# Kernel optimization log

Measured on AMD Instinct MI355X. Metric: run time of the kernel, lower is better.

## Reference

```python
import jax, jax.numpy as jnp
import numpy as np

N, C, SD, A, H = 1048576, 8192, 32, 4, 64


def _xavier(key, shape):
    fan_in, fan_out = shape
    lim = np.sqrt(6.0 / (fan_in + fan_out)).astype(np.float32)
    return jax.random.uniform(key, shape, jnp.float32, -lim, lim)


def setup_inputs() -> dict:
    key = jax.random.key(0)
    ks = jax.random.split(key, 10)
    return {
        "cell_state": jax.random.normal(ks[0], (N, SD), jnp.float32),
        "arch_state": jax.random.uniform(ks[1], (N, A), jnp.float32),
        "energy": jax.random.uniform(ks[2], (N,), jnp.float32),
        "phi_local": jax.random.uniform(ks[3], (N,), jnp.float32),
        "W1": _xavier(ks[4], (SD + A, H)),
        "b1": jnp.zeros((H,), jnp.float32),
        "W2": _xavier(ks[5], (H, 1)),
        "b2": jnp.zeros((1,), jnp.float32),
        "Wc1": _xavier(ks[6], (A + 3, H // 2)),
        "bc1": jnp.zeros((H // 2,), jnp.float32),
        "Wc2": _xavier(ks[7], (H // 2, 1)),
        "bc2": jnp.zeros((1,), jnp.float32),
        "segment_ids": jnp.sort(jax.random.randint(ks[8], (N,), 0, C, jnp.int32)),
        "n_clusters": C,
    }


def reference(cell_state, arch_state, energy, phi_local,
              W1, b1, W2, b2, Wc1, bc1, Wc2, bc2,
              segment_ids, n_clusters):
    seg = segment_ids
    nc = n_clusters
    seg_sum = lambda v: jax.ops.segment_sum(v, seg, num_segments=nc)

    # ---- cells -> clusters ----
    x = jnp.concatenate([cell_state, arch_state], axis=-1)          # [N, SD+A]
    h = jax.nn.relu(x @ W1 + b1)                                    # [N, H]
    base = jax.nn.sigmoid(h @ W2 + b2)[:, 0]                        # [N]
    importance = jnp.clip(base * energy * phi_local, 0.01, 1.0)
    w = importance * energy * phi_local                              # cell weight

    counts = seg_sum(jnp.ones_like(w))                               # [C]
    wsum = seg_sum(w)                                                # [C]
    safe_cnt = jnp.maximum(counts, 1.0)
    # normalized weights; uniform fallback when a cluster's weight sum is 0
    norm_w = jnp.where(wsum[seg] > 0,
                       w / jnp.maximum(wsum, 1e-30)[seg],
                       1.0 / safe_cnt[seg])
    aggregate = seg_sum(norm_w[:, None] * arch_state)                # [C, A]

    # unbiased per-dim variance averaged over dims (torch .var(dim=0).mean())
    mean = seg_sum(arch_state) / safe_cnt[:, None]                   # [C, A]
    sqdev = seg_sum((arch_state - mean[seg]) ** 2)                   # [C, A]
    var = jnp.where(counts >= 2.0,
                    sqdev.mean(-1) / jnp.maximum(counts - 1.0, 1.0),
                    0.0)                                             # [C]
    phi_cluster = 1.0 - jnp.minimum(1.0, var * 2.0)
    coherence = 1.0 - var

    # ---- clusters -> organism ----
    feats = jnp.concatenate([aggregate,
                             phi_cluster[:, None],
                             coherence[:, None],
                             jnp.minimum(1.0, counts / 20.0)[:, None]], axis=-1)  # [C, A+3]
    hc = jax.nn.relu(feats @ Wc1 + bc1)
    basec = jax.nn.sigmoid(hc @ Wc2 + bc2)[:, 0]                     # [C]
    impc = jnp.clip(basec * phi_cluster, 0.01, 1.0)
    valid = counts > 0
    wc = jnp.where(valid, impc * counts, 0.0)
    wc_sum = wc.sum()
    nvalid = jnp.maximum(valid.sum().astype(jnp.float32), 1.0)
    norm_wc = jnp.where(wc_sum > 0,
                        wc / jnp.maximum(wc_sum, 1e-30),
                        valid.astype(jnp.float32) / nvalid)
    global_archetype = (norm_wc[:, None] * aggregate).sum(0)         # [A]

    return aggregate, phi_cluster, coherence, global_archetype
```

## Files before the change

kernel.cpp:

```cpp
#include <hip/hip_runtime.h>
#include <hip/hip_bf16.h>

#define NC 8192
#define SDIM 32
#define ADIM 4
#define XDIM 36
#define HDIM 64
#define MLP_BLOCKS 1024

typedef _Float16 half8 __attribute__((ext_vector_type(8)));
typedef float f32x4 __attribute__((ext_vector_type(4)));

__device__ __forceinline__ float sigmoidf_(float t) {
    return 1.0f / (1.0f + __expf(-t));
}

__global__ __launch_bounds__(256) void bounds_kernel(
    const int* __restrict__ seg, int* __restrict__ startx,
    int* __restrict__ endx, int n)
{
    const int i = blockIdx.x * 256 + threadIdx.x;
    if (i >= n) return;
    const int s = seg[i];
    if (i == 0) {
        startx[s] = 0;
        for (int c = 0; c < s; ++c) { startx[c] = 0; endx[c] = 0; }
    } else {
        const int sp = seg[i - 1];
        if (sp != s) {
            startx[s] = i;
            for (int c = sp + 1; c < s; ++c) { startx[c] = i; endx[c] = i; }
        }
    }
    if (i == n - 1) {
        endx[s] = n;
        for (int c = s + 1; c < NC; ++c) { startx[c] = n; endx[c] = n; }
    } else if (seg[i + 1] != s) {
        endx[s] = i + 1;
    }
}

__global__ __launch_bounds__(256, 4) void mlp_kernel(
    const float* __restrict__ cell_state,
    const float* __restrict__ arch_state,
    const float* __restrict__ energy,
    const float* __restrict__ phi_local,
    const float* __restrict__ W1,
    const float* __restrict__ b1,
    const float* __restrict__ W2,
    const float* __restrict__ b2,
    float* __restrict__ w_out,
    int n)
{
    __shared__ half8 wpack[8 * 64];
    const int tid  = threadIdx.x;
    const int lane = tid & 63;
    const int l15  = lane & 15;
    const int lg   = lane >> 4;
    const int wv   = tid >> 6;

    #pragma unroll
    for (int fo = 0; fo < 2; ++fo) {
        const int f  = 2 * wv + fo;
        const int nt = f >> 1;
        const int s  = f & 1;
        half8 v = {};
        #pragma unroll
        for (int jj = 0; jj < 8; ++jj) {
            const int k = 32 * s + lg * 8 + jj;
            float wvv = 0.0f;
            if (k < XDIM)       wvv = W1[k * HDIM + 16 * nt + l15];
            else if (k == XDIM) wvv = b1[16 * nt + l15];
            v[jj] = (_Float16)wvv;
        }
        wpack[f * 64 + lane] = v;
    }
    __syncthreads();

    half8 af[4][2];
    #pragma unroll
    for (int nt = 0; nt < 4; ++nt)
        #pragma unroll
        for (int s = 0; s < 2; ++s)
            af[nt][s] = wpack[(nt * 2 + s) * 64 + lane];

    float w2v[16];
    #pragma unroll
    for (int nt = 0; nt < 4; ++nt)
        #pragma unroll
        for (int q = 0; q < 4; ++q)
            w2v[nt * 4 + q] = W2[16 * nt + lg * 4 + q];
    const float sb2 = b2[0];

    const int nch = (n + 63) >> 6;
    const int nw  = gridDim.x * 4;
    const int wid = blockIdx.x * 4 + wv;
    const int chw = (nch + nw - 1) / nw;

    #pragma unroll 1
    for (int j = 0; j < chw; ++j) {
        const int c = wid * chw + j;
        if (c >= nch) break;
        const int chunk_base = c * 64;

        float4 f0[4], f1[4];
        #pragma unroll
        for (int t = 0; t < 4; ++t) {
            int crow = chunk_base + 16 * t + l15;
            if (crow >= n) crow = n - 1;
            const float* cp = cell_state + (size_t)crow * SDIM + lg * 8;
            f0[t] = *reinterpret_cast<const float4*>(cp);
            f1[t] = *reinterpret_cast<const float4*>(cp + 4);
        }
        float4 a4[4];
        if (lg == 0) {
            #pragma unroll
            for (int t = 0; t < 4; ++t) {
                int crow = chunk_base + 16 * t + l15;
                if (crow >= n) crow = n - 1;
                a4[t] = reinterpret_cast<const float4*>(arch_state)[crow];
            }
        }
        const int gid = chunk_base + lane;
        const int lid = (gid < n) ? gid : (n - 1);
        const float e = energy[lid];
        const float p = phi_local[lid];

        float acc = 0.0f;
        #pragma unroll
        for (int t = 0; t < 4; ++t) {
            half8 x0;
            x0[0] = (_Float16)f0[t].x; x0[1] = (_Float16)f0[t].y;
            x0[2] = (_Float16)f0[t].z; x0[3] = (_Float16)f0[t].w;
            x0[4] = (_Float16)f1[t].x; x0[5] = (_Float16)f1[t].y;
            x0[6] = (_Float16)f1[t].z; x0[7] = (_Float16)f1[t].w;

            half8 x1 = {};
            if (lg == 0) {
                x1[0] = (_Float16)a4[t].x; x1[1] = (_Float16)a4[t].y;
                x1[2] = (_Float16)a4[t].z; x1[3] = (_Float16)a4[t].w;
                x1[4] = (_Float16)1.0f;
            }

            float pq = 0.0f;
            #pragma unroll
            for (int nt = 0; nt < 4; ++nt) {
                f32x4 cc = f32x4{0.f, 0.f, 0.f, 0.f};
                cc = __builtin_amdgcn_mfma_f32_16x16x32_f16(af[nt][0], x0, cc, 0, 0, 0);
                cc = __builtin_amdgcn_mfma_f32_16x16x32_f16(af[nt][1], x1, cc, 0, 0, 0);
                #pragma unroll
                for (int q = 0; q < 4; ++q)
                    pq = __builtin_fmaf(fmaxf(cc[q], 0.0f), w2v[nt * 4 + q], pq);
            }
            pq += __shfl_xor(pq, 16);
            pq += __shfl_xor(pq, 32);
            if (lg == t) acc = pq;
        }
        const float base = sigmoidf_(acc + sb2);

        if (gid < n) {
            const float ep = e * p;
            const float imp = fminf(fmaxf(base * ep, 0.01f), 1.0f);
            w_out[gid] = imp * ep;
        }
    }
}

__global__ __launch_bounds__(256) void cluster_kernel(
    const float* __restrict__ arch_state,
    const float* __restrict__ w_arr,
    const int*   __restrict__ startx,
    const int*   __restrict__ endx,
    const float* __restrict__ Wc1,
    const float* __restrict__ bc1,
    const float* __restrict__ Wc2,
    const float* __restrict__ bc2,
    float* __restrict__ out,
    float* __restrict__ ws2)
{
    const int lane = threadIdx.x & 63;
    const int c = blockIdx.x * 4 + (threadIdx.x >> 6);
    const int s0 = startx[c];
    const int e0 = endx[c];

    float pw = 0.0f;
    float pa0 = 0.f, pa1 = 0.f, pa2 = 0.f, pa3 = 0.f;
    float pw0 = 0.f, pw1 = 0.f, pw2 = 0.f, pw3 = 0.f;
    float pq0 = 0.f, pq1 = 0.f, pq2 = 0.f, pq3 = 0.f;
    const float4* arch4 = reinterpret_cast<const float4*>(arch_state);

    int i = s0 + lane;
    bool vcur = i < e0;
    float4 ac = {}; float wcur = 0.0f;
    if (vcur) { ac = arch4[i]; wcur = w_arr[i]; }
    while (vcur) {
        const int j = i + 64;
        const bool vnext = j < e0;
        float4 an = {}; float wnext = 0.0f;
        if (vnext) { an = arch4[j]; wnext = w_arr[j]; }
        pw += wcur;
        pa0 += ac.x; pa1 += ac.y; pa2 += ac.z; pa3 += ac.w;
        pw0 = __builtin_fmaf(wcur, ac.x, pw0); pw1 = __builtin_fmaf(wcur, ac.y, pw1);
        pw2 = __builtin_fmaf(wcur, ac.z, pw2); pw3 = __builtin_fmaf(wcur, ac.w, pw3);
        pq0 = __builtin_fmaf(ac.x, ac.x, pq0); pq1 = __builtin_fmaf(ac.y, ac.y, pq1);
        pq2 = __builtin_fmaf(ac.z, ac.z, pq2); pq3 = __builtin_fmaf(ac.w, ac.w, pq3);
        i = j; vcur = vnext; ac = an; wcur = wnext;
    }
#define RED13(F) F(pw) F(pa0) F(pa1) F(pa2) F(pa3) \
                 F(pw0) F(pw1) F(pw2) F(pw3) F(pq0) F(pq1) F(pq2) F(pq3)
#define BFLY(V) V += __shfl_xor(V, off_);
    #pragma unroll
    for (int off_ = 1; off_ < 64; off_ <<= 1) { RED13(BFLY) }

    const float cnt = (float)(e0 - s0);
    const float safe_cnt = fmaxf(cnt, 1.0f);
    const float wsum = pw;

    float agg[4];
    if (wsum > 0.0f) {
        const float inv = 1.0f / fmaxf(wsum, 1e-30f);
        agg[0] = pw0 * inv; agg[1] = pw1 * inv;
        agg[2] = pw2 * inv; agg[3] = pw3 * inv;
    } else {
        const float inv = 1.0f / safe_cnt;
        agg[0] = pa0 * inv; agg[1] = pa1 * inv;
        agg[2] = pa2 * inv; agg[3] = pa3 * inv;
    }

    const float sA[4]  = { pa0, pa1, pa2, pa3 };
    const float sA2[4] = { pq0, pq1, pq2, pq3 };
    float sq = 0.0f;
    #pragma unroll
    for (int d = 0; d < 4; ++d) {
        const float mean = sA[d] / safe_cnt;
        const float s2 = sA2[d] - 2.0f * mean * sA[d] + cnt * mean * mean;
        sq += fmaxf(s2, 0.0f);
    }
    const float var = (cnt >= 2.0f) ? (sq * 0.25f) / fmaxf(cnt - 1.0f, 1.0f) : 0.0f;
    const float phi_c = 1.0f - fminf(1.0f, var * 2.0f);
    const float coh = 1.0f - var;

    const float feats[7] = { agg[0], agg[1], agg[2], agg[3],
                             phi_c, coh, fminf(1.0f, cnt * 0.05f) };
    float t = bc2[0];
    #pragma unroll
    for (int j = 0; j < 32; ++j) {
        float hj = bc1[j];
        #pragma unroll
        for (int k = 0; k < 7; ++k)
            hj = __builtin_fmaf(feats[k], Wc1[k * 32 + j], hj);
        t += fmaxf(hj, 0.0f) * Wc2[j];
    }
    const float basec = sigmoidf_(t);
    const float impc = fminf(fmaxf(basec * phi_c, 0.01f), 1.0f);
    const bool valid = cnt > 0.0f;
    const float wc = valid ? impc * cnt : 0.0f;
    const float vf = valid ? 1.0f : 0.0f;

    if (lane == 0) {
        out[c * 4 + 0] = agg[0]; out[c * 4 + 1] = agg[1];
        out[c * 4 + 2] = agg[2]; out[c * 4 + 3] = agg[3];
        out[NC * 4 + c] = phi_c;
        out[NC * 5 + c] = coh;
        ws2[0 * NC + c] = wc;
        ws2[1 * NC + c] = vf;
        #pragma unroll
        for (int d = 0; d < 4; ++d) ws2[(2 + d) * NC + c] = wc * agg[d];
        #pragma unroll
        for (int d = 0; d < 4; ++d) ws2[(6 + d) * NC + c] = vf * agg[d];
    }
}

__global__ __launch_bounds__(1024) void finalize_kernel(
    const float* __restrict__ ws2, float* __restrict__ out)
{
    __shared__ float red[16][10];
    const int tid = threadIdx.x;
    const int lane = tid & 63;
    const int wv = tid >> 6;

    float r[10];
    #pragma unroll
    for (int k = 0; k < 10; ++k) r[k] = 0.0f;
    for (int c = tid; c < NC; c += 1024) {
        #pragma unroll
        for (int k = 0; k < 10; ++k) r[k] += ws2[k * NC + c];
    }
    #pragma unroll
    for (int off = 1; off < 64; off <<= 1) {
        #pragma unroll
        for (int k = 0; k < 10; ++k) r[k] += __shfl_xor(r[k], off);
    }
    if (lane == 0) {
        #pragma unroll
        for (int k = 0; k < 10; ++k) red[wv][k] = r[k];
    }
    __syncthreads();
    if (tid == 0) {
        float g[10];
        #pragma unroll
        for (int k = 0; k < 10; ++k) {
            float acc = 0.0f;
            for (int i = 0; i < 16; ++i) acc += red[i][k];
            g[k] = acc;
        }
        const float wcs = g[0];
        const float nv = fmaxf(g[1], 1.0f);
        #pragma unroll
        for (int d = 0; d < 4; ++d) {
            out[NC * 6 + d] = (wcs > 0.0f) ? g[2 + d] / fmaxf(wcs, 1e-30f)
                                           : g[6 + d] / nv;
        }
    }
}

extern "C" void kernel_launch(void* const* d_in, const int* in_sizes, int n_in,
                              void* d_out, int out_size, void* d_ws, size_t ws_size,
                              hipStream_t stream) {
    const float* cell_state = (const float*)d_in[0];
    const float* arch_state = (const float*)d_in[1];
    const float* energy     = (const float*)d_in[2];
    const float* phi_local  = (const float*)d_in[3];
    const float* W1  = (const float*)d_in[4];
    const float* b1  = (const float*)d_in[5];
    const float* W2  = (const float*)d_in[6];
    const float* b2  = (const float*)d_in[7];
    const float* Wc1 = (const float*)d_in[8];
    const float* bc1 = (const float*)d_in[9];
    const float* Wc2 = (const float*)d_in[10];
    const float* bc2 = (const float*)d_in[11];
    const int* seg   = (const int*)d_in[12];

    const int n = in_sizes[2];
    float* out = (float*)d_out;

    float* w_arr = (float*)d_ws;
    int* startx  = (int*)(w_arr + n);
    int* endx    = startx + NC;
    float* ws2   = (float*)(endx + NC);

    bounds_kernel<<<(n + 255) / 256, 256, 0, stream>>>(seg, startx, endx, n);
    mlp_kernel<<<MLP_BLOCKS, 256, 0, stream>>>(cell_state, arch_state, energy,
                                               phi_local, W1, b1, W2, b2,
                                               w_arr, n);
    cluster_kernel<<<NC / 4, 256, 0, stream>>>(arch_state, w_arr, startx, endx,
                                               Wc1, bc1, Wc2, bc2, out, ws2);
    finalize_kernel<<<1, 1024, 0, stream>>>(ws2, out);
}
```

Measured before the change: 64.61 us.

## Issue loads for two MLP chunks before computing to overlap memory latency

The MLP loop now loads the inputs of two 64-row chunks up front and then runs the MFMA compute on each, so more memory requests are in flight per wave. Occupancy hint drops from 4 to 3 blocks per CU to make room for the doubled register footprint. The per-wave chunk assignment is hardcoded to 4 chunks (two iterations of two), which assumes the grid size times 4 waves times 4 chunks covers all chunks; with 1024 blocks and 16384 chunks this holds exactly.

```diff
diff --git a/kernel.cpp b/kernel.cpp
--- a/kernel.cpp
+++ b/kernel.cpp
@@ -40,7 +40,70 @@
     }
 }
 
-__global__ __launch_bounds__(256, 4) void mlp_kernel(
+__device__ __forceinline__ void issue_loads(
+    int chunk_base, int n, int l15, int lg, int lane,
+    const float* __restrict__ cell_state, const float* __restrict__ arch_state,
+    const float* __restrict__ energy, const float* __restrict__ phi_local,
+    float4 (&f0)[4], float4 (&f1)[4], float4 (&a4)[4], float& e, float& p)
+{
+    #pragma unroll
+    for (int t = 0; t < 4; ++t) {
+        int crow = chunk_base + 16 * t + l15;
+        if (crow >= n) crow = n - 1;
+        const float* cp = cell_state + (size_t)crow * SDIM + lg * 8;
+        f0[t] = *reinterpret_cast<const float4*>(cp);
+        f1[t] = *reinterpret_cast<const float4*>(cp + 4);
+    }
+    if (lg == 0) {
+        #pragma unroll
+        for (int t = 0; t < 4; ++t) {
+            int crow = chunk_base + 16 * t + l15;
+            if (crow >= n) crow = n - 1;
+            a4[t] = reinterpret_cast<const float4*>(arch_state)[crow];
+        }
+    }
+    int gid = chunk_base + lane; if (gid >= n) gid = n - 1;
+    e = energy[gid]; p = phi_local[gid];
+}
+
+__device__ __forceinline__ float compute_chunk(
+    const float4 (&f0)[4], const float4 (&f1)[4], const float4 (&a4)[4],
+    const half8 (&af)[4][2], const float (&w2v)[16], int lg)
+{
+    float acc = 0.0f;
+    #pragma unroll
+    for (int t = 0; t < 4; ++t) {
+        half8 x0;
+        x0[0] = (_Float16)f0[t].x; x0[1] = (_Float16)f0[t].y;
+        x0[2] = (_Float16)f0[t].z; x0[3] = (_Float16)f0[t].w;
+        x0[4] = (_Float16)f1[t].x; x0[5] = (_Float16)f1[t].y;
+        x0[6] = (_Float16)f1[t].z; x0[7] = (_Float16)f1[t].w;
+
+        half8 x1 = {};
+        if (lg == 0) {
+            x1[0] = (_Float16)a4[t].x; x1[1] = (_Float16)a4[t].y;
+            x1[2] = (_Float16)a4[t].z; x1[3] = (_Float16)a4[t].w;
+            x1[4] = (_Float16)1.0f;
+        }
+
+        float pq = 0.0f;
+        #pragma unroll
+        for (int nt = 0; nt < 4; ++nt) {
+            f32x4 cc = f32x4{0.f, 0.f, 0.f, 0.f};
+            cc = __builtin_amdgcn_mfma_f32_16x16x32_f16(af[nt][0], x0, cc, 0, 0, 0);
+            cc = __builtin_amdgcn_mfma_f32_16x16x32_f16(af[nt][1], x1, cc, 0, 0, 0);
+            #pragma unroll
+            for (int q = 0; q < 4; ++q)
+                pq = __builtin_fmaf(fmaxf(cc[q], 0.0f), w2v[nt * 4 + q], pq);
+        }
+        pq += __shfl_xor(pq, 16);
+        pq += __shfl_xor(pq, 32);
+        if (lg == t) acc = pq;
+    }
+    return acc;
+}
+
+__global__ __launch_bounds__(256, 3) void mlp_kernel(
     const float* __restrict__ cell_state,
     const float* __restrict__ arch_state,
     const float* __restrict__ energy,
@@ -93,75 +156,40 @@
     const float sb2 = b2[0];
 
     const int nch = (n + 63) >> 6;
-    const int nw  = gridDim.x * 4;
     const int wid = blockIdx.x * 4 + wv;
-    const int chw = (nch + nw - 1) / nw;
 
     #pragma unroll 1
-    for (int j = 0; j < chw; ++j) {
-        const int c = wid * chw + j;
-        if (c >= nch) break;
-        const int chunk_base = c * 64;
-
-        float4 f0[4], f1[4];
-        #pragma unroll
-        for (int t = 0; t < 4; ++t) {
-            int crow = chunk_base + 16 * t + l15;
-            if (crow >= n) crow = n - 1;
-            const float* cp = cell_state + (size_t)crow * SDIM + lg * 8;
-            f0[t] = *reinterpret_cast<const float4*>(cp);
-            f1[t] = *reinterpret_cast<const float4*>(cp + 4);
-        }
-        float4 a4[4];
-        if (lg == 0) {
-            #pragma unroll
-            for (int t = 0; t < 4; ++t) {
-                int crow = chunk_base + 16 * t + l15;
-                if (crow >= n) crow = n - 1;
-                a4[t] = reinterpret_cast<const float4*>(arch_state)[crow];
+    for (int j = 0; j < 2; ++j) {
+        const int c0 = wid * 4 + 2 * j;
+        const int c1 = c0 + 1;
+        if (c0 >= nch) break;
+
+        float4 f0A[4], f1A[4], a4A[4]; float eA, pA;
+        issue_loads(c0 * 64, n, l15, lg, lane, cell_state, arch_state,
+                    energy, phi_local, f0A, f1A, a4A, eA, pA);
+        const bool hasB = c1 < nch;
+        float4 f0B[4], f1B[4], a4B[4]; float eB = 0.f, pB = 0.f;
+        if (hasB)
+            issue_loads(c1 * 64, n, l15, lg, lane, cell_state, arch_state,
+                        energy, phi_local, f0B, f1B, a4B, eB, pB);
+
+        {
+            const float base = sigmoidf_(compute_chunk(f0A, f1A, a4A, af, w2v, lg) + sb2);
+            const int gid = c0 * 64 + lane;
+            if (gid < n) {
+                const float ep = eA * pA;
+                const float imp = fminf(fmaxf(base * ep, 0.01f), 1.0f);
+                w_out[gid] = imp * ep;
             }
         }
-        const int gid = chunk_base + lane;
-        const int lid = (gid < n) ? gid : (n - 1);
-        const float e = energy[lid];
-        const float p = phi_local[lid];
-
-        float acc = 0.0f;
-        #pragma unroll
-        for (int t = 0; t < 4; ++t) {
-            half8 x0;
-            x0[0] = (_Float16)f0[t].x; x0[1] = (_Float16)f0[t].y;
-            x0[2] = (_Float16)f0[t].z; x0[3] = (_Float16)f0[t].w;
-            x0[4] = (_Float16)f1[t].x; x0[5] = (_Float16)f1[t].y;
-            x0[6] = (_Float16)f1[t].z; x0[7] = (_Float16)f1[t].w;
-
-            half8 x1 = {};
-            if (lg == 0) {
-                x1[0] = (_Float16)a4[t].x; x1[1] = (_Float16)a4[t].y;
-                x1[2] = (_Float16)a4[t].z; x1[3] = (_Float16)a4[t].w;
-                x1[4] = (_Float16)1.0f;
+        if (hasB) {
+            const float base = sigmoidf_(compute_chunk(f0B, f1B, a4B, af, w2v, lg) + sb2);
+            const int gid = c1 * 64 + lane;
+            if (gid < n) {
+                const float ep = eB * pB;
+                const float imp = fminf(fmaxf(base * ep, 0.01f), 1.0f);
+                w_out[gid] = imp * ep;
             }
-
-            float pq = 0.0f;
-            #pragma unroll
-            for (int nt = 0; nt < 4; ++nt) {
-                f32x4 cc = f32x4{0.f, 0.f, 0.f, 0.f};
-                cc = __builtin_amdgcn_mfma_f32_16x16x32_f16(af[nt][0], x0, cc, 0, 0, 0);
-                cc = __builtin_amdgcn_mfma_f32_16x16x32_f16(af[nt][1], x1, cc, 0, 0, 0);
-                #pragma unroll
-                for (int q = 0; q < 4; ++q)
-                    pq = __builtin_fmaf(fmaxf(cc[q], 0.0f), w2v[nt * 4 + q], pq);
-            }
-            pq += __shfl_xor(pq, 16);
-            pq += __shfl_xor(pq, 32);
-            if (lg == t) acc = pq;
-        }
-        const float base = sigmoidf_(acc + sb2);
-
-        if (gid < n) {
-            const float ep = e * p;
-            const float imp = fminf(fmaxf(base * ep, 0.01f), 1.0f);
-            w_out[gid] = imp * ep;
         }
     }
 }
```

Measured after the change: 82.32 us. 27.4% more time.

## Stage MLP input tile through LDS with coalesced loads and fp16 conversion

Applied to the files above, without the earlier changes.

The MLP kernel now loads a 256-row tile of cell_state and arch_state with fully coalesced float4 loads, converts it to fp16 and writes it into padded shared memory. Waves then read MFMA operands from LDS. Work is distributed in block-strided 256-row tiles instead of per-wave contiguous chunks. This aims to replace the strided per-lane global loads with coalesced ones, at the cost of two barriers per tile and extra LDS traffic, which may reduce overlap of loads with compute.

```diff
diff --git a/kernel.cpp b/kernel.cpp
--- a/kernel.cpp
+++ b/kernel.cpp
@@ -9,6 +9,7 @@
 #define MLP_BLOCKS 1024
 
 typedef _Float16 half8 __attribute__((ext_vector_type(8)));
+typedef _Float16 half4 __attribute__((ext_vector_type(4)));
 typedef float f32x4 __attribute__((ext_vector_type(4)));
 
 __device__ __forceinline__ float sigmoidf_(float t) {
@@ -52,6 +53,7 @@
     float* __restrict__ w_out,
     int n)
 {
+    __shared__ _Float16 xs[256 * 40];
     __shared__ half8 wpack[8 * 64];
     const int tid  = threadIdx.x;
     const int lane = tid & 63;
@@ -92,55 +94,48 @@
             w2v[nt * 4 + q] = W2[16 * nt + lg * 4 + q];
     const float sb2 = b2[0];
 
-    const int nch = (n + 63) >> 6;
-    const int nw  = gridDim.x * 4;
-    const int wid = blockIdx.x * 4 + wv;
-    const int chw = (nch + nw - 1) / nw;
+    const float4* cell4 = reinterpret_cast<const float4*>(cell_state);
+    const float4* arch4 = reinterpret_cast<const float4*>(arch_state);
 
     #pragma unroll 1
-    for (int j = 0; j < chw; ++j) {
-        const int c = wid * chw + j;
-        if (c >= nch) break;
-        const int chunk_base = c * 64;
-
-        float4 f0[4], f1[4];
+    for (int cb = blockIdx.x * 256; cb < n; cb += gridDim.x * 256) {
+        __syncthreads();
+
+        #pragma unroll
+        for (int uu = 0; uu < 8; ++uu) {
+            const int u   = uu * 256 + tid;
+            const int row = u >> 3;
+            const int c4  = u & 7;
+            float4 v = {0.f, 0.f, 0.f, 0.f};
+            if (cb + row < n) v = cell4[(size_t)cb * 8 + u];
+            half4 h;
+            h[0] = (_Float16)v.x; h[1] = (_Float16)v.y;
+            h[2] = (_Float16)v.z; h[3] = (_Float16)v.w;
+            *reinterpret_cast<half4*>(&xs[row * 40 + c4 * 4]) = h;
+        }
+        {
+            const int row = tid;
+            float4 a = {0.f, 0.f, 0.f, 0.f};
+            if (cb + row < n) a = arch4[cb + row];
+            half4 h;
+            h[0] = (_Float16)a.x; h[1] = (_Float16)a.y;
+            h[2] = (_Float16)a.z; h[3] = (_Float16)a.w;
+            *reinterpret_cast<half4*>(&xs[row * 40 + 32]) = h;
+            half4 hb;
+            hb[0] = (_Float16)1.0f; hb[1] = (_Float16)0.0f;
+            hb[2] = (_Float16)0.0f; hb[3] = (_Float16)0.0f;
+            *reinterpret_cast<half4*>(&xs[row * 40 + 36]) = hb;
+        }
+        __syncthreads();
+
+        float acc = 0.0f;
         #pragma unroll
         for (int t = 0; t < 4; ++t) {
-            int crow = chunk_base + 16 * t + l15;
-            if (crow >= n) crow = n - 1;
-            const float* cp = cell_state + (size_t)crow * SDIM + lg * 8;
-            f0[t] = *reinterpret_cast<const float4*>(cp);
-            f1[t] = *reinterpret_cast<const float4*>(cp + 4);
-        }
-        float4 a4[4];
-        if (lg == 0) {
-            #pragma unroll
-            for (int t = 0; t < 4; ++t) {
-                int crow = chunk_base + 16 * t + l15;
-                if (crow >= n) crow = n - 1;
-                a4[t] = reinterpret_cast<const float4*>(arch_state)[crow];
-            }
-        }
-        const int gid = chunk_base + lane;
-        const int lid = (gid < n) ? gid : (n - 1);
-        const float e = energy[lid];
-        const float p = phi_local[lid];
-
-        float acc = 0.0f;
-        #pragma unroll
-        for (int t = 0; t < 4; ++t) {
-            half8 x0;
-            x0[0] = (_Float16)f0[t].x; x0[1] = (_Float16)f0[t].y;
-            x0[2] = (_Float16)f0[t].z; x0[3] = (_Float16)f0[t].w;
-            x0[4] = (_Float16)f1[t].x; x0[5] = (_Float16)f1[t].y;
-            x0[6] = (_Float16)f1[t].z; x0[7] = (_Float16)f1[t].w;
-
+            const int r = wv * 64 + 16 * t + l15;
+            const half8 x0 = *reinterpret_cast<const half8*>(&xs[r * 40 + lg * 8]);
             half8 x1 = {};
-            if (lg == 0) {
-                x1[0] = (_Float16)a4[t].x; x1[1] = (_Float16)a4[t].y;
-                x1[2] = (_Float16)a4[t].z; x1[3] = (_Float16)a4[t].w;
-                x1[4] = (_Float16)1.0f;
-            }
+            if (lg == 0)
+                x1 = *reinterpret_cast<const half8*>(&xs[r * 40 + 32]);
 
             float pq = 0.0f;
             #pragma unroll
@@ -158,8 +153,9 @@
         }
         const float base = sigmoidf_(acc + sb2);
 
+        const int gid = cb + wv * 64 + lane;
         if (gid < n) {
-            const float ep = e * p;
+            const float ep = energy[gid] * phi_local[gid];
             const float imp = fminf(fmaxf(base * ep, 0.01f), 1.0f);
             w_out[gid] = imp * ep;
         }
```

After: 64.58 us. About the same (-0.0%).
